# Kernel tuning notes

Measured on AMD Instinct MI355X. Metric: run time of the kernel, lower is better.

Reference implementation:

```python
import jax, jax.numpy as jnp
import numpy as np

NEG_SLOPE = 0.2  # PyG GATConv default negative_slope
H, C = 4, 64     # heads, per-head channels


def gat_layer(x, src, dst, edge_attr, W, a_src, a_dst, We, a_e, b):
    """PyG-style GATConv with edge features, concat=True. src/dst include self loops."""
    N = x.shape[0]
    h = (x @ W).reshape(N, H, C)                      # [N,H,C]
    al_s = (h * a_src[None]).sum(-1)                  # [N,H]
    al_d = (h * a_dst[None]).sum(-1)                  # [N,H]
    eh = (edge_attr @ We).reshape(-1, H, C)           # [E,H,C]
    al_e = (eh * a_e[None]).sum(-1)                   # [E,H]
    alpha = jax.nn.leaky_relu(al_s[src] + al_d[dst] + al_e, NEG_SLOPE)  # [E,H]
    # softmax over incoming edges of each destination node
    m = jax.ops.segment_max(alpha, dst, num_segments=N)
    p = jnp.exp(alpha - m[dst])
    denom = jax.ops.segment_sum(p, dst, num_segments=N)
    w = p / (denom[dst] + 1e-16)                      # [E,H]
    msg = h[src] * w[..., None]                       # [E,H,C]
    out = jax.ops.segment_sum(msg, dst, num_segments=N)  # [N,H,C]
    return out.reshape(N, H * C) + b


def setup_inputs() -> dict:
    key = jax.random.key(0)
    ks = jax.random.split(key, 20)
    N, E = 50000, 800000
    s = 0.05
    inp = {
        'x': jax.random.normal(ks[0], (N, 5), jnp.float32),
        'edge_index': jax.random.randint(ks[1], (2, E), 0, N, jnp.int32),
        'edge_attr': jax.random.normal(ks[2], (E, 4), jnp.float32),
        'W0': jax.random.normal(ks[3], (5, 256), jnp.float32) * s,
        'a_src0': jax.random.normal(ks[4], (H, C), jnp.float32) * s,
        'a_dst0': jax.random.normal(ks[5], (H, C), jnp.float32) * s,
        'We0': jax.random.normal(ks[6], (4, 256), jnp.float32) * s,
        'a_e0': jax.random.normal(ks[7], (H, C), jnp.float32) * s,
        'b0': jnp.zeros((256,), jnp.float32),
        'W1': jax.random.normal(ks[8], (256, 256), jnp.float32) * s,
        'a_src1': jax.random.normal(ks[9], (H, C), jnp.float32) * s,
        'a_dst1': jax.random.normal(ks[10], (H, C), jnp.float32) * s,
        'We1': jax.random.normal(ks[11], (4, 256), jnp.float32) * s,
        'a_e1': jax.random.normal(ks[12], (H, C), jnp.float32) * s,
        'b1': jnp.zeros((256,), jnp.float32),
        'Wm1': jax.random.normal(ks[13], (768, 128), jnp.float32) * s,
        'bm1': jnp.zeros((128,), jnp.float32),
        'Wm2': jax.random.normal(ks[14], (128, 64), jnp.float32) * s,
        'bm2': jnp.zeros((64,), jnp.float32),
        'Wm3': jax.random.normal(ks[15], (64, 128), jnp.float32) * s,
        'bm3': jnp.zeros((128,), jnp.float32),
    }
    return inp


def reference(x, edge_index, edge_attr,
              W0, a_src0, a_dst0, We0, a_e0, b0,
              W1, a_src1, a_dst1, We1, a_e1, b1,
              Wm1, bm1, Wm2, bm2, Wm3, bm3):
    N = x.shape[0]
    # add self loops once; self-loop edge_attr = mean of edge_attr (PyG fill_value='mean')
    loops = jnp.arange(N, dtype=edge_index.dtype)
    src = jnp.concatenate([edge_index[0], loops])
    dst = jnp.concatenate([edge_index[1], loops])
    mean_ea = jnp.mean(edge_attr, axis=0, keepdims=True)
    ea = jnp.concatenate([edge_attr, jnp.broadcast_to(mean_ea, (N, edge_attr.shape[1]))], axis=0)

    h = gat_layer(x, src, dst, ea, W0, a_src0, a_dst0, We0, a_e0, b0)
    h = jax.nn.relu(h)  # dropout is identity in eval
    h = gat_layer(h, src, dst, ea, W1, a_src1, a_dst1, We1, a_e1, b1)

    mean_pool = jnp.mean(h, axis=0)                      # [256]
    max_pool = jnp.max(h, axis=0)                        # [256]
    att = jax.nn.softmax(jnp.sum(h * mean_pool[None], axis=1))  # [N]
    att_pool = jnp.sum(h * att[:, None], axis=0)         # [256]
    comb = jnp.concatenate([mean_pool, max_pool, att_pool])  # [768]

    z = jax.nn.relu(comb @ Wm1 + bm1)
    z = jax.nn.relu(z @ Wm2 + bm2)
    g = z @ Wm3 + bm3
    return g[None]  # [1,128]
```

## Files before the change

kernel.cpp:

```cpp
#include <hip/hip_runtime.h>
#include <hip/hip_fp16.h>
#include <type_traits>

static const long long N_ = 50000;
static const long long E_ = 800000;
static const int NCOPY = 8;
#define LOG2E 1.44269504088896f

typedef __attribute__((ext_vector_type(8))) short bf16x8;
typedef __attribute__((ext_vector_type(4))) float f32x4;

__device__ __forceinline__ float lrelu(float x){ return x >= 0.f ? x : 0.2f*x; }
__device__ __forceinline__ unsigned fkey(float x){
  unsigned u = __float_as_uint(x);
  return (u & 0x80000000u) ? ~u : (u | 0x80000000u);
}
__device__ __forceinline__ float unfkey(unsigned k){
  return __uint_as_float((k & 0x80000000u) ? (k & 0x7fffffffu) : ~k);
}
__device__ __forceinline__ unsigned h2u(__half2 h){ return *(unsigned*)&h; }

__global__ void k_pre(const int* __restrict__ ei, int* __restrict__ deg8,
                      unsigned char* __restrict__ rank,
                      const float* __restrict__ ea, float* __restrict__ sum_ea,
                      const float* __restrict__ W1, ushort* __restrict__ Bhi,
                      ushort* __restrict__ Blo){
  int t = threadIdx.x;
  long long e = (long long)blockIdx.x*256 + t;
  if (e < E_){
    int d = ei[E_ + e];
    int copy = blockIdx.x & (NCOPY-1);
    int old = atomicAdd(&deg8[copy*(int)N_ + d], 1);
    rank[e] = (unsigned char)old;
  }
  if (blockIdx.x < 256){
    int k = blockIdx.x, n = t;
    float v = W1[k*256+n];
    unsigned u = __float_as_uint(v);
    ushort hi = (ushort)(u>>16);
    float rem = v - __uint_as_float(u & 0xffff0000u);
    unsigned ur = __float_as_uint(rem);
    ushort lo = (ushort)((ur + 0x7fff + ((ur>>16)&1)) >> 16);
    int tl = n>>4, kb = k>>5, q = (k>>3)&3, j = k&7;
    long long idx = ((((long long)tl*8+kb)*64 + q*16 + (n&15))<<3) + j;
    Bhi[idx] = hi; Blo[idx] = lo;
  }
  __shared__ float lds[256];
  float s = 0.f;
  for (long long i = (long long)blockIdx.x*256 + t; i < E_*4; i += (long long)gridDim.x*256)
    s += ea[i];
  lds[t] = s; __syncthreads();
  for (int st=128; st>=4; st>>=1){ if (t<st) lds[t] += lds[t+st]; __syncthreads(); }
  if (t<4) atomicAdd(&sum_ea[t], lds[t]);
}

__global__ void k_scan1(const int* __restrict__ deg8, int* __restrict__ bsum){
  __shared__ int lds[256];
  int t = threadIdx.x;
  long long idx = (long long)blockIdx.x*256 + t;
  int v = 0;
  if (idx < N_){
    #pragma unroll
    for (int c=0;c<NCOPY;c++) v += deg8[c*(int)N_ + idx];
  }
  lds[t] = v;
  __syncthreads();
  for (int st=128; st>=1; st>>=1){ if (t<st) lds[t] += lds[t+st]; __syncthreads(); }
  if (t==0) bsum[blockIdx.x] = lds[0];
}

__global__ void k_scan2(const int* __restrict__ bsum, int* __restrict__ bpre, int nb,
                        int* __restrict__ rowptr,
                        const float* __restrict__ We0, const float* __restrict__ ae0,
                        const float* __restrict__ We1, const float* __restrict__ ae1,
                        const float* __restrict__ sum_ea, float* __restrict__ small){
  __shared__ int lds[256];
  int t = threadIdx.x;
  int v = (t < nb) ? bsum[t] : 0;
  lds[t] = v; __syncthreads();
  for (int off=1; off<256; off<<=1){
    int add = (t>=off) ? lds[t-off] : 0;
    __syncthreads();
    lds[t] += add;
    __syncthreads();
  }
  if (t < nb) bpre[t] = lds[t] - v;
  if (t == 0) rowptr[N_] = (int)E_;
  if (t < 32){
    int l = t>>4, f = (t>>2)&3, h = t&3;
    const float* We = l ? We1 : We0;
    const float* ae = l ? ae1 : ae0;
    float s = 0.f;
    for (int cc=0; cc<64; cc++) s += We[f*256 + h*64 + cc]*ae[h*64+cc];
    small[l*16 + f*4 + h] = s * LOG2E;
  }
  __syncthreads();
  if (t < 8){
    int l = t>>2, h = t&3;
    const float* Ae = small + l*16;
    const float invE = 1.f/(float)E_;
    float s = 0.f;
    for (int f=0; f<4; f++) s += sum_ea[f]*invE*Ae[f*4+h];
    small[32 + l*4 + h] = s;
  }
}

__global__ void k_scan3(const int* __restrict__ deg8, const int* __restrict__ bpre,
                        int* __restrict__ rowptr, int* __restrict__ base){
  __shared__ int lds[256];
  int t = threadIdx.x;
  long long idx = (long long)blockIdx.x*256 + t;
  int dd[NCOPY]; int v = 0;
  if (idx < N_){
    #pragma unroll
    for (int c=0;c<NCOPY;c++){ dd[c] = deg8[c*(int)N_ + idx]; v += dd[c]; }
  }
  lds[t] = v; __syncthreads();
  for (int off=1; off<256; off<<=1){
    int add = (t>=off) ? lds[t-off] : 0;
    __syncthreads();
    lds[t] += add;
    __syncthreads();
  }
  if (idx < N_){
    int rp = bpre[blockIdx.x] + lds[t] - v;
    rowptr[idx] = rp;
    int cum = rp;
    #pragma unroll
    for (int c=0;c<NCOPY;c++){ base[c*(int)N_ + idx] = cum; cum += dd[c]; }
  }
}

__global__ void k_h0(const float* __restrict__ x, const float* __restrict__ W0,
                     const float* __restrict__ as0, const float* __restrict__ ad0,
                     __half* __restrict__ h0, float* __restrict__ als, float* __restrict__ ald){
  int wid = (int)(((long long)blockIdx.x*blockDim.x + threadIdx.x) >> 6);
  int lane = threadIdx.x & 63;
  if (wid >= (int)N_) return;
  const float* xr = x + wid*5;
  float xv[5];
  #pragma unroll
  for (int f=0; f<5; f++) xv[f] = xr[f];
  int c = lane*4;
  float a0=0,a1=0,a2=0,a3=0;
  #pragma unroll
  for (int f=0; f<5; f++){
    const float* wr = W0 + f*256 + c;
    a0 += xv[f]*wr[0]; a1 += xv[f]*wr[1]; a2 += xv[f]*wr[2]; a3 += xv[f]*wr[3];
  }
  uint2 pk = make_uint2(h2u(__floats2half2_rn(a0,a1)), h2u(__floats2half2_rn(a2,a3)));
  *(uint2*)(h0 + wid*256 + c) = pk;
  const float* asp = as0 + c;
  const float* adp = ad0 + c;
  float ss = a0*asp[0]+a1*asp[1]+a2*asp[2]+a3*asp[3];
  float dd = a0*adp[0]+a1*adp[1]+a2*adp[2]+a3*adp[3];
  int head = lane>>4;
  #pragma unroll
  for (int m=1; m<16; m<<=1){ ss += __shfl_xor(ss, m); dd += __shfl_xor(dd, m); }
  if ((lane&15)==0){ als[wid*4+head]=ss*LOG2E; ald[wid*4+head]=dd*LOG2E; }
}

__global__ void k_scatter(const int* __restrict__ ei, const float* __restrict__ ea,
                          const int* __restrict__ base, const unsigned char* __restrict__ rank,
                          int2* __restrict__ csr2, uint4* __restrict__ pe,
                          const float* __restrict__ small,
                          const float* __restrict__ als0, const float* __restrict__ ald0){
  long long e = (long long)blockIdx.x*256 + threadIdx.x;
  if (e >= E_) return;
  int s = ei[e], d = ei[E_+e];
  int copy = blockIdx.x & (NCOPY-1);
  int pos = base[copy*(int)N_ + d] + (int)rank[e];
  csr2[pos] = make_int2(s, d);
  float4 v = *(const float4*)(ea + e*4);
  float4 As = *(const float4*)(als0 + s*4);
  float4 Ad = *(const float4*)(ald0 + d*4);
  float as_[4] = {As.x,As.y,As.z,As.w};
  float ad_[4] = {Ad.x,Ad.y,Ad.z,Ad.w};
  float p0[4], o1[4];
  #pragma unroll
  for (int h=0; h<4; h++){
    float a0 = v.x*small[0+h]  + v.y*small[4+h]  + v.z*small[8+h]  + v.w*small[12+h];
    p0[h] = exp2f(lrelu(as_[h] + ad_[h] + a0));
    o1[h] = v.x*small[16+h] + v.y*small[20+h] + v.z*small[24+h] + v.w*small[28+h];
  }
  uint4 pk = make_uint4(h2u(__floats2half2_rn(p0[0],p0[1])),
                        h2u(__floats2half2_rn(p0[2],p0[3])),
                        h2u(__floats2half2_rn(o1[0],o1[1])),
                        h2u(__floats2half2_rn(o1[2],o1[3])));
  pe[pos] = pk;
}

__global__ void k_palpha1(const int2* __restrict__ csr2, const uint4* __restrict__ pe,
                          const float* __restrict__ als1, const float* __restrict__ ald1,
                          __half* __restrict__ p1h){
  long long i = (long long)blockIdx.x*256 + threadIdx.x;
  if (i >= E_) return;
  int2 sd = csr2[i];
  float4 As = *(const float4*)(als1 + sd.x*4);
  float4 Ad = *(const float4*)(ald1 + sd.y*4);
  uint4 pk = pe[i];
  float2 e01 = __half22float2(*(__half2*)&pk.z);
  float2 e23 = __half22float2(*(__half2*)&pk.w);
  float p0 = exp2f(lrelu(As.x+Ad.x+e01.x));
  float p1 = exp2f(lrelu(As.y+Ad.y+e01.y));
  float p2 = exp2f(lrelu(As.z+Ad.z+e23.x));
  float p3 = exp2f(lrelu(As.w+Ad.w+e23.y));
  uint2 o = make_uint2(h2u(__floats2half2_rn(p0,p1)), h2u(__floats2half2_rn(p2,p3)));
  *(uint2*)(p1h + i*4) = o;
}

template<typename OutT, bool RELU>
__global__ __launch_bounds__(256) void k_agg(const __half* __restrict__ hin,
    const float* __restrict__ als, const float* __restrict__ ald,
    const int* __restrict__ rowptr, const int2* __restrict__ csr2,
    const __half* __restrict__ ph, int pstride,
    const float* __restrict__ small, int loop_off,
    const float* __restrict__ bias, OutT* __restrict__ out){
  int wid = (int)(((long long)blockIdx.x*256 + threadIdx.x) >> 6);
  int lane = threadIdx.x & 63;
  if (wid >= (int)N_) return;
  int half_ = lane>>5, l5 = lane&31;
  int head = l5>>3, c8 = l5*8;
  const uint4* hp = (const uint4*)hin;
  float a[8]; float den;
  {
    float pS = exp2f(lrelu(als[wid*4+head] + ald[wid*4+head] + small[loop_off+head]));
    float pp = (half_==0) ? pS : 0.f;
    uint4 r = hp[wid*32 + l5];
    float2 f0 = __half22float2(*(__half2*)&r.x);
    float2 f1 = __half22float2(*(__half2*)&r.y);
    float2 f2 = __half22float2(*(__half2*)&r.z);
    float2 f3 = __half22float2(*(__half2*)&r.w);
    den = pp;
    a[0]=pp*f0.x; a[1]=pp*f0.y; a[2]=pp*f1.x; a[3]=pp*f1.y;
    a[4]=pp*f2.x; a[5]=pp*f2.y; a[6]=pp*f3.x; a[7]=pp*f3.y;
  }
  int beg = rowptr[wid], end = rowptr[wid+1];
  int i = beg;
  for (; i+7 < end; i += 8){
    int   sv[4]; float pv[4]; uint4 rr[4];
    #pragma unroll
    for (int k=0;k<4;k++){
      int e = i + 2*k + half_;
      sv[k] = csr2[e].x;
      pv[k] = __half2float(ph[e*pstride + head]);
    }
    #pragma unroll
    for (int k=0;k<4;k++) rr[k] = hp[sv[k]*32 + l5];
    #pragma unroll
    for (int k=0;k<4;k++){
      float2 f0 = __half22float2(*(__half2*)&rr[k].x);
      float2 f1 = __half22float2(*(__half2*)&rr[k].y);
      float2 f2 = __half22float2(*(__half2*)&rr[k].z);
      float2 f3 = __half22float2(*(__half2*)&rr[k].w);
      float p = pv[k];
      den += p;
      a[0]+=p*f0.x; a[1]+=p*f0.y; a[2]+=p*f1.x; a[3]+=p*f1.y;
      a[4]+=p*f2.x; a[5]+=p*f2.y; a[6]+=p*f3.x; a[7]+=p*f3.y;
    }
  }
  for (; i < end; i += 2){
    int e = i + half_;
    bool act = (e < end);
    int ee = act ? e : (end-1);
    int s0 = csr2[ee].x;
    float p = act ? __half2float(ph[ee*pstride + head]) : 0.f;
    uint4 r = hp[s0*32 + l5];
    float2 f0 = __half22float2(*(__half2*)&r.x);
    float2 f1 = __half22float2(*(__half2*)&r.y);
    float2 f2 = __half22float2(*(__half2*)&r.z);
    float2 f3 = __half22float2(*(__half2*)&r.w);
    den += p;
    a[0]+=p*f0.x; a[1]+=p*f0.y; a[2]+=p*f1.x; a[3]+=p*f1.y;
    a[4]+=p*f2.x; a[5]+=p*f2.y; a[6]+=p*f3.x; a[7]+=p*f3.y;
  }
  den += __shfl_xor(den, 32);
  #pragma unroll
  for (int j=0;j<8;j++) a[j] += __shfl_xor(a[j], 32);
  if (half_ == 0){
    float inv = 1.f/(den + 1e-16f);
    float4 b0 = *(const float4*)(bias + c8);
    float4 b1 = *(const float4*)(bias + c8 + 4);
    float o[8];
    o[0]=a[0]*inv+b0.x; o[1]=a[1]*inv+b0.y; o[2]=a[2]*inv+b0.z; o[3]=a[3]*inv+b0.w;
    o[4]=a[4]*inv+b1.x; o[5]=a[5]*inv+b1.y; o[6]=a[6]*inv+b1.z; o[7]=a[7]*inv+b1.w;
    if (RELU){
      #pragma unroll
      for (int j=0;j<8;j++) o[j] = fmaxf(o[j], 0.f);
    }
    if constexpr (std::is_same<OutT,__half>::value){
      uint4 qk = make_uint4(h2u(__floats2half2_rn(o[0],o[1])), h2u(__floats2half2_rn(o[2],o[3])),
                            h2u(__floats2half2_rn(o[4],o[5])), h2u(__floats2half2_rn(o[6],o[7])));
      *(uint4*)(out + wid*256 + c8) = qk;
    } else {
      *(float4*)(out + wid*256 + c8)     = make_float4(o[0],o[1],o[2],o[3]);
      *(float4*)(out + wid*256 + c8 + 4) = make_float4(o[4],o[5],o[6],o[7]);
    }
  }
}

__global__ __launch_bounds__(256) void k_gemm(const float* __restrict__ A,
    const ushort* __restrict__ Bhi, const ushort* __restrict__ Blo,
    __half* __restrict__ Ch, const float* __restrict__ as1, const float* __restrict__ ad1,
    float* __restrict__ als, float* __restrict__ ald){
  __shared__ ushort Ah[32*264];
  __shared__ ushort Al[32*264];
  int t = threadIdx.x;
  long long base = (long long)blockIdx.x*32;
  for (int i=t; i<2048; i+=256){
    int r = i>>6, q4 = i&63;
    float4 v = make_float4(0.f,0.f,0.f,0.f);
    if (base + r < N_) v = *(const float4*)(A + (base+r)*256 + q4*4);
    float vv[4] = {v.x,v.y,v.z,v.w};
    ushort hh[4], ll[4];
    #pragma unroll
    for (int e=0;e<4;e++){
      unsigned u = __float_as_uint(vv[e]);
      hh[e] = (ushort)(u>>16);
      float rem = vv[e] - __uint_as_float(u & 0xffff0000u);
      unsigned ur = __float_as_uint(rem);
      ll[e] = (ushort)((ur + 0x7fff + ((ur>>16)&1)) >> 16);
    }
    int off = r*264 + q4*4;
    *(ushort4*)(Ah+off) = make_ushort4(hh[0],hh[1],hh[2],hh[3]);
    *(ushort4*)(Al+off) = make_ushort4(ll[0],ll[1],ll[2],ll[3]);
  }
  __syncthreads();
  int w = t>>6, lane = t&63, m = lane&15, q = lane>>4;
  int rbase = (w>>1)*16;
  int nhalf = (w&1)*8;
  f32x4 acc[8];
  #pragma unroll
  for (int i=0;i<8;i++) acc[i] = (f32x4){0.f,0.f,0.f,0.f};
  for (int kb=0; kb<8; kb++){
    int aoff = (rbase+m)*264 + kb*32 + q*8;
    bf16x8 ah = *(const bf16x8*)(Ah + aoff);
    bf16x8 al = *(const bf16x8*)(Al + aoff);
    #pragma unroll
    for (int tt=0; tt<8; tt++){
      long long bidx = ((((long long)(nhalf+tt)*8+kb)*64 + lane)<<3);
      bf16x8 bh = *(const bf16x8*)(Bhi + bidx);
      bf16x8 bl = *(const bf16x8*)(Blo + bidx);
      acc[tt] = __builtin_amdgcn_mfma_f32_16x16x32_bf16(ah, bh, acc[tt], 0,0,0);
      acc[tt] = __builtin_amdgcn_mfma_f32_16x16x32_bf16(al, bh, acc[tt], 0,0,0);
      acc[tt] = __builtin_amdgcn_mfma_f32_16x16x32_bf16(ah, bl, acc[tt], 0,0,0);
    }
  }
  float ssv[4][2], ddv[4][2];
  #pragma unroll
  for (int r=0;r<4;r++){ ssv[r][0]=0.f; ssv[r][1]=0.f; ddv[r][0]=0.f; ddv[r][1]=0.f; }
  #pragma unroll
  for (int tt=0; tt<8; tt++){
    int col = (nhalf+tt)*16 + m;
    float as_ = as1[col], ad_ = ad1[col];
    int hh = tt>>2;
    #pragma unroll
    for (int r=0;r<4;r++){
      ssv[r][hh] += acc[tt][r]*as_;
      ddv[r][hh] += acc[tt][r]*ad_;
    }
  }
  #pragma unroll
  for (int r=0;r<4;r++){
    #pragma unroll
    for (int hh=0; hh<2; hh++){
      #pragma unroll
      for (int mm=1; mm<16; mm<<=1){
        ssv[r][hh] += __shfl_xor(ssv[r][hh], mm);
        ddv[r][hh] += __shfl_xor(ddv[r][hh], mm);
      }
    }
  }
  #pragma unroll
  for (int r=0;r<4;r++){
    long long grow = base + rbase + q*4 + r;
    if (grow < N_){
      #pragma unroll
      for (int tt=0; tt<8; tt++)
        Ch[grow*256 + (nhalf+tt)*16 + m] = __float2half(acc[tt][r]);
      if (m==0){
        int hb = (w&1)*2;
        als[grow*4 + hb+0] = ssv[r][0]*LOG2E;
        ald[grow*4 + hb+0] = ddv[r][0]*LOG2E;
        als[grow*4 + hb+1] = ssv[r][1]*LOG2E;
        ald[grow*4 + hb+1] = ddv[r][1]*LOG2E;
      }
    }
  }
}

__global__ void k_pool1(const __half* __restrict__ h2, float* __restrict__ sum_pool,
                        unsigned* __restrict__ maxkey){
  int c = threadIdx.x;
  float s = 0.f; float m = -3.4e38f;
  for (long long n = blockIdx.x; n < N_; n += gridDim.x){
    float v = __half2float(h2[n*256+c]); s += v; m = fmaxf(m, v);
  }
  atomicAdd(&sum_pool[c], s);
  atomicMax(&maxkey[c], fkey(m));
}

__global__ void k_atts(const __half* __restrict__ h2, const float* __restrict__ sum_pool,
                       float* __restrict__ sarr, float* __restrict__ ssum){
  __shared__ float lsum[4];
  int t = threadIdx.x; int lane = t&63; int w = t>>6;
  const float invN = 1.f/(float)N_;
  int c = lane*4;
  float4 mp = *(const float4*)(sum_pool + c);
  float esum = 0.f;
  for (long long wid = (long long)blockIdx.x*4 + w; wid < N_; wid += (long long)gridDim.x*4){
    uint2 pk = *(const uint2*)(h2 + wid*256 + c);
    float2 a01 = __half22float2(*(__half2*)&pk.x);
    float2 a23 = __half22float2(*(__half2*)&pk.y);
    float s = (a01.x*mp.x + a01.y*mp.y + a23.x*mp.z + a23.y*mp.w)*invN;
    #pragma unroll
    for (int m=1; m<64; m<<=1) s += __shfl_xor(s, m);
    if (lane==0){ sarr[wid] = s; esum += __expf(s); }
  }
  if (lane==0) lsum[w] = esum;
  __syncthreads();
  if (t==0) atomicAdd(ssum, lsum[0]+lsum[1]+lsum[2]+lsum[3]);
}

__global__ void k_attp(const __half* __restrict__ h2, const float* __restrict__ sarr,
                       const float* __restrict__ ssum, float* __restrict__ att_pool){
  int c = threadIdx.x;
  float inv = 1.f/(*ssum);
  float acc = 0.f;
  for (long long n = blockIdx.x; n < N_; n += gridDim.x){
    float w = __expf(sarr[n])*inv;
    acc += __half2float(h2[n*256+c])*w;
  }
  atomicAdd(&att_pool[c], acc);
}

__global__ void k_mlp(const float* __restrict__ sum_pool, const unsigned* __restrict__ maxkey,
                      const float* __restrict__ att_pool,
                      const float* __restrict__ Wm1, const float* __restrict__ bm1,
                      const float* __restrict__ Wm2, const float* __restrict__ bm2,
                      const float* __restrict__ Wm3, const float* __restrict__ bm3,
                      float* __restrict__ out){
  __shared__ float comb[768];
  __shared__ float z1p[4][128]; __shared__ float z1[128];
  __shared__ float z2p[8][64];  __shared__ float z2[64];
  __shared__ float z3p[4][128];
  int t = threadIdx.x;
  const float invN = 1.f/(float)N_;
  for (int i=t; i<768; i+=512){
    float v;
    if (i < 256)      v = sum_pool[i]*invN;
    else if (i < 512) v = unfkey(maxkey[i-256]);
    else              v = att_pool[i-512];
    comb[i] = v;
  }
  __syncthreads();
  { int n = t&127, part = t>>7;
    float a = 0.f;
    for (int f=part*192; f<part*192+192; f++) a += comb[f]*Wm1[f*128+n];
    z1p[part][n] = a;
  }
  __syncthreads();
  if (t < 128)
    z1[t] = fmaxf(bm1[t] + z1p[0][t]+z1p[1][t]+z1p[2][t]+z1p[3][t], 0.f);
  __syncthreads();
  { int n = t&63, part = t>>6;
    float a = 0.f;
    for (int f=part*16; f<part*16+16; f++) a += z1[f]*Wm2[f*64+n];
    z2p[part][n] = a;
  }
  __syncthreads();
  if (t < 64){
    float a = bm2[t];
    #pragma unroll
    for (int p=0;p<8;p++) a += z2p[p][t];
    z2[t] = fmaxf(a, 0.f);
  }
  __syncthreads();
  { int n = t&127, part = t>>7;
    float a = 0.f;
    for (int f=part*16; f<part*16+16; f++) a += z2[f]*Wm3[f*128+n];
    z3p[part][n] = a;
  }
  __syncthreads();
  if (t < 128)
    out[t] = bm3[t] + z3p[0][t]+z3p[1][t]+z3p[2][t]+z3p[3][t];
}

extern "C" void kernel_launch(void* const* d_in, const int* in_sizes, int n_in,
                              void* d_out, int out_size, void* d_ws, size_t ws_size,
                              hipStream_t stream){
  (void)in_sizes; (void)n_in; (void)out_size; (void)ws_size;
  const float* x   = (const float*)d_in[0];
  const int*   ei  = (const int*)d_in[1];
  const float* ea  = (const float*)d_in[2];
  const float* W0  = (const float*)d_in[3];
  const float* as0 = (const float*)d_in[4];
  const float* ad0 = (const float*)d_in[5];
  const float* We0 = (const float*)d_in[6];
  const float* ae0 = (const float*)d_in[7];
  const float* b0  = (const float*)d_in[8];
  const float* W1  = (const float*)d_in[9];
  const float* as1 = (const float*)d_in[10];
  const float* ad1 = (const float*)d_in[11];
  const float* We1 = (const float*)d_in[12];
  const float* ae1 = (const float*)d_in[13];
  const float* b1  = (const float*)d_in[14];
  const float* Wm1 = (const float*)d_in[15];
  const float* bm1 = (const float*)d_in[16];
  const float* Wm2 = (const float*)d_in[17];
  const float* bm2 = (const float*)d_in[18];
  const float* Wm3 = (const float*)d_in[19];
  const float* bm3 = (const float*)d_in[20];
  float* out = (float*)d_out;

  char* ws = (char*)d_ws;
  size_t o = 0;
  auto alloc = [&](size_t bytes)->size_t{
    size_t r = o; o = (o + bytes + 255) & ~(size_t)255; return r;
  };
  size_t o_bufF   = alloc((size_t)N_*256*4);
  size_t o_bufH   = alloc((size_t)N_*256*2);
  size_t o_als0   = alloc((size_t)N_*4*4);
  size_t o_ald0   = alloc((size_t)N_*4*4);
  size_t o_als1   = alloc((size_t)N_*4*4);
  size_t o_ald1   = alloc((size_t)N_*4*4);
  size_t o_rowptr = alloc((size_t)(N_+1)*4);
  size_t o_csr2   = alloc((size_t)E_*8);
  size_t o_pe     = alloc((size_t)E_*16);
  size_t o_p1     = alloc((size_t)E_*4*2);
  size_t o_rank   = alloc((size_t)E_);
  size_t o_base   = alloc((size_t)NCOPY*N_*4);
  size_t o_sarr   = alloc((size_t)N_*4);
  size_t o_Bhi    = alloc((size_t)256*256*2);
  size_t o_Blo    = alloc((size_t)256*256*2);
  size_t o_bsum   = alloc(256*4);
  size_t o_bpre   = alloc(256*4);
  size_t zstart   = o;
  size_t o_deg8   = alloc((size_t)NCOPY*N_*4);
  size_t o_sumea  = alloc(16);
  size_t o_sumpool= alloc(256*4);
  size_t o_maxkey = alloc(256*4);
  size_t o_attpool= alloc(256*4);
  size_t o_ssum   = alloc(4);
  size_t zend     = o;
  size_t o_small  = alloc(40*4);

  float*  bufF   = (float*)(ws + o_bufF);
  __half* bufH   = (__half*)(ws + o_bufH);
  __half* h2h    = (__half*)(ws + o_bufF);
  float* pals0  = (float*)(ws + o_als0);
  float* pald0  = (float*)(ws + o_ald0);
  float* pals1  = (float*)(ws + o_als1);
  float* pald1  = (float*)(ws + o_ald1);
  int*   rowptr = (int*)(ws + o_rowptr);
  int2*  csr2   = (int2*)(ws + o_csr2);
  uint4* pe     = (uint4*)(ws + o_pe);
  __half* p1h   = (__half*)(ws + o_p1);
  unsigned char* rank = (unsigned char*)(ws + o_rank);
  int*   base   = (int*)(ws + o_base);
  float* sarr   = (float*)(ws + o_sarr);
  ushort* Bhi   = (ushort*)(ws + o_Bhi);
  ushort* Blo   = (ushort*)(ws + o_Blo);
  int*   bsum   = (int*)(ws + o_bsum);
  int*   bpre   = (int*)(ws + o_bpre);
  int*   deg8   = (int*)(ws + o_deg8);
  float* sumea  = (float*)(ws + o_sumea);
  float* sumpool= (float*)(ws + o_sumpool);
  unsigned* maxkey = (unsigned*)(ws + o_maxkey);
  float* attpool= (float*)(ws + o_attpool);
  float* ssum   = (float*)(ws + o_ssum);
  float* small  = (float*)(ws + o_small);

  hipMemsetAsync(ws + zstart, 0, zend - zstart, stream);

  int eb = (int)((E_ + 255)/256);
  int nb_wave = (int)((N_*64 + 255)/256);
  int gb = (int)((N_ + 31)/32);
  int sb = (int)((N_ + 255)/256);

  k_pre    <<<eb, 256, 0, stream>>>(ei, deg8, rank, ea, sumea, W1, Bhi, Blo);
  k_scan1  <<<sb, 256, 0, stream>>>(deg8, bsum);
  k_scan2  <<<1, 256, 0, stream>>>(bsum, bpre, sb, rowptr,
                                   We0, ae0, We1, ae1, sumea, small);
  k_scan3  <<<sb, 256, 0, stream>>>(deg8, bpre, rowptr, base);
  k_h0     <<<nb_wave, 256, 0, stream>>>(x, W0, as0, ad0, bufH, pals0, pald0);
  k_scatter<<<eb, 256, 0, stream>>>(ei, ea, base, rank, csr2, pe,
                                    small, pals0, pald0);
  k_agg<float,true>  <<<nb_wave, 256, 0, stream>>>(bufH, pals0, pald0, rowptr, csr2,
                                         (const __half*)pe, 8, small, 32, b0, bufF);
  k_gemm   <<<gb, 256, 0, stream>>>(bufF, Bhi, Blo, bufH, as1, ad1, pals1, pald1);
  k_palpha1<<<eb, 256, 0, stream>>>(csr2, pe, pals1, pald1, p1h);
  k_agg<__half,false><<<nb_wave, 256, 0, stream>>>(bufH, pals1, pald1, rowptr, csr2,
                                         p1h, 4, small, 36, b1, h2h);
  k_pool1  <<<256, 256, 0, stream>>>(h2h, sumpool, maxkey);
  k_atts   <<<1024, 256, 0, stream>>>(h2h, sumpool, sarr, ssum);
  k_attp   <<<256, 256, 0, stream>>>(h2h, sarr, ssum, attpool);
  k_mlp    <<<1, 512, 0, stream>>>(sumpool, maxkey, attpool,
                                   Wm1, bm1, Wm2, bm2, Wm3, bm3, out);
}
```

Measured before the change: 533.6 us.

## Fuse attention-pool passes into one kernel and move edge-attr mean into scan

The attention pooling previously ran two passes over the node features: one for scores and the softmax denominator, another to form the weighted sum. It now makes a single pass that accumulates exp(score)*h and the exp sum together, and normalizes inside the MLP kernel. This drops one read of the N×256 half buffer, the per-node score array and a launch. The edge_attr mean reduction also moves from a grid-wide atomic in k_pre to per-block partials in k_scan1, which k_scan2 sums serially; the unstabilized exp (no max subtraction) matches the prior code.

```diff
diff --git a/kernel.cpp b/kernel.cpp
--- a/kernel.cpp
+++ b/kernel.cpp
@@ -22,7 +22,6 @@
 
 __global__ void k_pre(const int* __restrict__ ei, int* __restrict__ deg8,
                       unsigned char* __restrict__ rank,
-                      const float* __restrict__ ea, float* __restrict__ sum_ea,
                       const float* __restrict__ W1, ushort* __restrict__ Bhi,
                       ushort* __restrict__ Blo){
   int t = threadIdx.x;
@@ -45,17 +44,12 @@
     long long idx = ((((long long)tl*8+kb)*64 + q*16 + (n&15))<<3) + j;
     Bhi[idx] = hi; Blo[idx] = lo;
   }
-  __shared__ float lds[256];
-  float s = 0.f;
-  for (long long i = (long long)blockIdx.x*256 + t; i < E_*4; i += (long long)gridDim.x*256)
-    s += ea[i];
-  lds[t] = s; __syncthreads();
-  for (int st=128; st>=4; st>>=1){ if (t<st) lds[t] += lds[t+st]; __syncthreads(); }
-  if (t<4) atomicAdd(&sum_ea[t], lds[t]);
-}
-
-__global__ void k_scan1(const int* __restrict__ deg8, int* __restrict__ bsum){
+}
+
+__global__ void k_scan1(const int* __restrict__ deg8, int* __restrict__ bsum,
+                        const float* __restrict__ ea, float* __restrict__ eapart){
   __shared__ int lds[256];
+  __shared__ float fl[256];
   int t = threadIdx.x;
   long long idx = (long long)blockIdx.x*256 + t;
   int v = 0;
@@ -64,17 +58,27 @@
     for (int c=0;c<NCOPY;c++) v += deg8[c*(int)N_ + idx];
   }
   lds[t] = v;
-  __syncthreads();
-  for (int st=128; st>=1; st>>=1){ if (t<st) lds[t] += lds[t+st]; __syncthreads(); }
+  float s = 0.f;
+  for (long long i = (long long)blockIdx.x*256 + t; i < E_*4; i += (long long)gridDim.x*256)
+    s += ea[i];
+  fl[t] = s;
+  __syncthreads();
+  for (int st=128; st>=1; st>>=1){
+    if (t<st) lds[t] += lds[t+st];
+    if (t<st && st>=4) fl[t] += fl[t+st];
+    __syncthreads();
+  }
   if (t==0) bsum[blockIdx.x] = lds[0];
+  if (t<4) eapart[blockIdx.x*4 + t] = fl[t];
 }
 
 __global__ void k_scan2(const int* __restrict__ bsum, int* __restrict__ bpre, int nb,
                         int* __restrict__ rowptr,
                         const float* __restrict__ We0, const float* __restrict__ ae0,
                         const float* __restrict__ We1, const float* __restrict__ ae1,
-                        const float* __restrict__ sum_ea, float* __restrict__ small){
+                        const float* __restrict__ eapart, float* __restrict__ small){
   __shared__ int lds[256];
+  __shared__ float sea[4];
   int t = threadIdx.x;
   int v = (t < nb) ? bsum[t] : 0;
   lds[t] = v; __syncthreads();
@@ -86,6 +90,11 @@
   }
   if (t < nb) bpre[t] = lds[t] - v;
   if (t == 0) rowptr[N_] = (int)E_;
+  if (t < 4){
+    float s = 0.f;
+    for (int b=0;b<nb;b++) s += eapart[b*4+t];
+    sea[t] = s;
+  }
   if (t < 32){
     int l = t>>4, f = (t>>2)&3, h = t&3;
     const float* We = l ? We1 : We0;
@@ -100,7 +109,7 @@
     const float* Ae = small + l*16;
     const float invE = 1.f/(float)E_;
     float s = 0.f;
-    for (int f=0; f<4; f++) s += sum_ea[f]*invE*Ae[f*4+h];
+    for (int f=0; f<4; f++) s += sea[f]*invE*Ae[f*4+h];
     small[32 + l*4 + h] = s;
   }
 }
@@ -401,13 +410,15 @@
 }
 
 __global__ void k_atts(const __half* __restrict__ h2, const float* __restrict__ sum_pool,
-                       float* __restrict__ sarr, float* __restrict__ ssum){
-  __shared__ float lsum[4];
+                       float* __restrict__ ssum, float* __restrict__ att_raw){
+  __shared__ float part[4][256];
+  __shared__ float es[4];
   int t = threadIdx.x; int lane = t&63; int w = t>>6;
   const float invN = 1.f/(float)N_;
   int c = lane*4;
   float4 mp = *(const float4*)(sum_pool + c);
   float esum = 0.f;
+  float acc0=0.f, acc1=0.f, acc2=0.f, acc3=0.f;
   for (long long wid = (long long)blockIdx.x*4 + w; wid < N_; wid += (long long)gridDim.x*4){
     uint2 pk = *(const uint2*)(h2 + wid*256 + c);
     float2 a01 = __half22float2(*(__half2*)&pk.x);
@@ -415,27 +426,22 @@
     float s = (a01.x*mp.x + a01.y*mp.y + a23.x*mp.z + a23.y*mp.w)*invN;
     #pragma unroll
     for (int m=1; m<64; m<<=1) s += __shfl_xor(s, m);
-    if (lane==0){ sarr[wid] = s; esum += __expf(s); }
-  }
-  if (lane==0) lsum[w] = esum;
-  __syncthreads();
-  if (t==0) atomicAdd(ssum, lsum[0]+lsum[1]+lsum[2]+lsum[3]);
-}
-
-__global__ void k_attp(const __half* __restrict__ h2, const float* __restrict__ sarr,
-                       const float* __restrict__ ssum, float* __restrict__ att_pool){
-  int c = threadIdx.x;
-  float inv = 1.f/(*ssum);
-  float acc = 0.f;
-  for (long long n = blockIdx.x; n < N_; n += gridDim.x){
-    float w = __expf(sarr[n])*inv;
-    acc += __half2float(h2[n*256+c])*w;
-  }
-  atomicAdd(&att_pool[c], acc);
+    float e = __expf(s);
+    if (lane==0) esum += e;
+    acc0 += e*a01.x; acc1 += e*a01.y; acc2 += e*a23.x; acc3 += e*a23.y;
+  }
+  part[w][c+0]=acc0; part[w][c+1]=acc1; part[w][c+2]=acc2; part[w][c+3]=acc3;
+  if (lane==0) es[w] = esum;
+  __syncthreads();
+  if (t < 256){
+    float v = part[0][t]+part[1][t]+part[2][t]+part[3][t];
+    atomicAdd(&att_raw[t], v);
+  }
+  if (t==0) atomicAdd(ssum, es[0]+es[1]+es[2]+es[3]);
 }
 
 __global__ void k_mlp(const float* __restrict__ sum_pool, const unsigned* __restrict__ maxkey,
-                      const float* __restrict__ att_pool,
+                      const float* __restrict__ att_raw, const float* __restrict__ ssum,
                       const float* __restrict__ Wm1, const float* __restrict__ bm1,
                       const float* __restrict__ Wm2, const float* __restrict__ bm2,
                       const float* __restrict__ Wm3, const float* __restrict__ bm3,
@@ -446,11 +452,12 @@
   __shared__ float z3p[4][128];
   int t = threadIdx.x;
   const float invN = 1.f/(float)N_;
+  float invS = 1.f/(*ssum);
   for (int i=t; i<768; i+=512){
     float v;
     if (i < 256)      v = sum_pool[i]*invN;
     else if (i < 512) v = unfkey(maxkey[i-256]);
-    else              v = att_pool[i-512];
+    else              v = att_raw[i-512]*invS;
     comb[i] = v;
   }
   __syncthreads();
@@ -530,17 +537,16 @@
   size_t o_p1     = alloc((size_t)E_*4*2);
   size_t o_rank   = alloc((size_t)E_);
   size_t o_base   = alloc((size_t)NCOPY*N_*4);
-  size_t o_sarr   = alloc((size_t)N_*4);
   size_t o_Bhi    = alloc((size_t)256*256*2);
   size_t o_Blo    = alloc((size_t)256*256*2);
   size_t o_bsum   = alloc(256*4);
   size_t o_bpre   = alloc(256*4);
+  size_t o_eapart = alloc(256*4*4);
   size_t zstart   = o;
   size_t o_deg8   = alloc((size_t)NCOPY*N_*4);
-  size_t o_sumea  = alloc(16);
   size_t o_sumpool= alloc(256*4);
   size_t o_maxkey = alloc(256*4);
-  size_t o_attpool= alloc(256*4);
+  size_t o_attraw = alloc(256*4);
   size_t o_ssum   = alloc(4);
   size_t zend     = o;
   size_t o_small  = alloc(40*4);
@@ -558,16 +564,15 @@
   __half* p1h   = (__half*)(ws + o_p1);
   unsigned char* rank = (unsigned char*)(ws + o_rank);
   int*   base   = (int*)(ws + o_base);
-  float* sarr   = (float*)(ws + o_sarr);
   ushort* Bhi   = (ushort*)(ws + o_Bhi);
   ushort* Blo   = (ushort*)(ws + o_Blo);
   int*   bsum   = (int*)(ws + o_bsum);
   int*   bpre   = (int*)(ws + o_bpre);
+  float* eapart = (float*)(ws + o_eapart);
   int*   deg8   = (int*)(ws + o_deg8);
-  float* sumea  = (float*)(ws + o_sumea);
   float* sumpool= (float*)(ws + o_sumpool);
   unsigned* maxkey = (unsigned*)(ws + o_maxkey);
-  float* attpool= (float*)(ws + o_attpool);
+  float* attraw = (float*)(ws + o_attraw);
   float* ssum   = (float*)(ws + o_ssum);
   float* small  = (float*)(ws + o_small);
 
@@ -578,10 +583,10 @@
   int gb = (int)((N_ + 31)/32);
   int sb = (int)((N_ + 255)/256);
 
-  k_pre    <<<eb, 256, 0, stream>>>(ei, deg8, rank, ea, sumea, W1, Bhi, Blo);
-  k_scan1  <<<sb, 256, 0, stream>>>(deg8, bsum);
+  k_pre    <<<eb, 256, 0, stream>>>(ei, deg8, rank, W1, Bhi, Blo);
+  k_scan1  <<<sb, 256, 0, stream>>>(deg8, bsum, ea, eapart);
   k_scan2  <<<1, 256, 0, stream>>>(bsum, bpre, sb, rowptr,
-                                   We0, ae0, We1, ae1, sumea, small);
+                                   We0, ae0, We1, ae1, eapart, small);
   k_scan3  <<<sb, 256, 0, stream>>>(deg8, bpre, rowptr, base);
   k_h0     <<<nb_wave, 256, 0, stream>>>(x, W0, as0, ad0, bufH, pals0, pald0);
   k_scatter<<<eb, 256, 0, stream>>>(ei, ea, base, rank, csr2, pe,
@@ -593,8 +598,7 @@
   k_agg<__half,false><<<nb_wave, 256, 0, stream>>>(bufH, pals1, pald1, rowptr, csr2,
                                          p1h, 4, small, 36, b1, h2h);
   k_pool1  <<<256, 256, 0, stream>>>(h2h, sumpool, maxkey);
-  k_atts   <<<1024, 256, 0, stream>>>(h2h, sumpool, sarr, ssum);
-  k_attp   <<<256, 256, 0, stream>>>(h2h, sarr, ssum, attpool);
-  k_mlp    <<<1, 512, 0, stream>>>(sumpool, maxkey, attpool,
+  k_atts   <<<256, 256, 0, stream>>>(h2h, sumpool, ssum, attraw);
+  k_mlp    <<<1, 512, 0, stream>>>(sumpool, maxkey, attraw, ssum,
                                    Wm1, bm1, Wm2, bm2, Wm3, bm3, out);
 }
```

Result: faster. 494.9 us (-7.3%).
